# Kernel optimization log

Measured on AMD Instinct MI355X. Metric: run time of the kernel, lower is better.

## Reference

```python
import math
import jax, jax.numpy as jnp
import numpy as np

N_ORDERS = 2
CHUNK = 64  # tokens per chunk (before virtual-token expansion)


def _expand_derivative(x, n):
    """expand_virtual_tokens(mode='derivative'): [B,H,S,D] -> [B,H,S*n,D]."""
    B, H, S, D = x.shape
    pad = jnp.zeros((B, H, n - 1, D), x.dtype)
    xp = jnp.concatenate([pad, x], axis=2)  # [B,H,S+n-1,D]
    coeffs = np.array([(-1) ** kk * math.comb(n - 1, kk) for kk in range(n)], dtype=np.float32)
    coeffs = coeffs / np.abs(coeffs).sum()  # L1-normalized binomial coeffs
    # window j at token t is x_pad[t+j]*coeffs[j]; then flip window dim (as in torch .flip(-1))
    win = jnp.stack([xp[:, :, j:j + S, :] * coeffs[j] for j in range(n)], axis=3)  # [B,H,S,n,D]
    win = win[:, :, :, ::-1, :]
    return win.reshape(B, H, S * n, D)


def _unlinear(x, scale=2.0):
    """unlinear_activation: gated norm-scaled gelu applied to inter-chunk state."""
    xn = jnp.linalg.norm(x, axis=-1, keepdims=True) + 1e-6
    return x / scale * jax.nn.gelu(scale * x / xn, approximate=True)


def _stab(x):
    # ensure_stability: clamp to [-1e4, 1e4], nan -> center (0)
    return jnp.nan_to_num(jnp.clip(x, -1e4, 1e4), nan=0.0, posinf=1e4, neginf=-1e4)


def _forward(q, k, v, beta):
    n = N_ORDERS
    B, H, S, D = q.shape
    qe = _expand_derivative(q, n)
    ke = _expand_derivative(k, n)
    ve = _expand_derivative(v, n)
    be = jnp.repeat(beta, n, axis=-1)[..., None]  # [B,H,S*n,1]
    w = ke * be  # delta-rule write keys
    u = ve * be  # delta-rule write values

    Cn = CHUNK * n                     # virtual tokens per chunk
    NC = (S * n) // Cn                 # number of chunks
    ch = lambda x: x.reshape(B, H, NC, Cn, D)
    qc, kc, wc, uc = ch(qe), ch(ke), ch(w), ch(u)

    # triangular (forward-substitution) inversion per chunk:
    # T = (I + tril(W K^T, -1))^{-1}  == fast_invert_matrix of the strictly-lower system
    A = jnp.tril(jnp.einsum('bhnid,bhnjd->bhnij', wc, kc), -1)
    eye = jnp.eye(Cn, dtype=q.dtype)
    T = jax.scipy.linalg.solve_triangular(
        eye + A, jnp.broadcast_to(eye, A.shape), lower=True, unit_diagonal=True)
    wci = jnp.einsum('bhnij,bhnjd->bhnid', T, wc)
    uci = jnp.einsum('bhnij,bhnjd->bhnid', T, uc)

    def chunk_step(h, xs):
        # sequential_delta_product_scan body: per-token Householder updates, n_orders steps
        qx, wx, ux = xs  # each [B,H,Cn,D]
        C = CHUNK
        qr = qx.reshape(B, H, C, n, D)
        wr = wx.reshape(B, H, C, n, D)
        ur = ux.reshape(B, H, C, n, D)
        state = jnp.broadcast_to(h[:, :, None], (B, H, C, D, D))  # per-token state
        outs = []
        for s in range(n):
            qs, ws, us = qr[:, :, :, s], wr[:, :, :, s], ur[:, :, :, s]
            kho = jnp.einsum('bhcd,bhcde->bhce', ws, state)
            uval = us - kho
            o_inter = jnp.einsum('bhcd,bhcde->bhce', qs, state)
            o_intra = qs * uval
            state = _stab(state + jnp.einsum('bhcd,bhce->bhcde', ws, uval))
            outs.append(o_intra + o_inter)
        o = jnp.stack(outs, axis=3).reshape(B, H, C * n, D)  # interleave: pos t*n+s
        h_new = _unlinear(state[:, :, -1])  # linear_activation=False path
        return h_new, o

    xs = (jnp.moveaxis(qc, 2, 0), jnp.moveaxis(wci, 2, 0), jnp.moveaxis(uci, 2, 0))
    h0 = jnp.zeros((B, H, D, D), q.dtype)
    _, os = jax.lax.scan(chunk_step, h0, xs)  # os: [NC,B,H,Cn,D]
    out_v = jnp.moveaxis(os, 0, 2).reshape(B, H, S, n, D)
    return out_v[..., n - 1, :]  # collapse virtual tokens: keep last-order output per token


def setup_inputs() -> dict:
    key = jax.random.key(0)
    kq, kk, kv, kb = jax.random.split(key, 4)
    B, H, S, D = 2, 16, 2048, 64
    return {
        'q': jax.random.normal(kq, (B, H, S, D), jnp.float32),
        'k': jax.random.normal(kk, (B, H, S, D), jnp.float32),
        'v': jax.random.normal(kv, (B, H, S, D), jnp.float32),
        'beta': jax.random.uniform(kb, (B, H, S), jnp.float32),
    }


def reference(q, k, v, beta):
    return _forward(q, k, v, beta)
```

## Files before the change

kernel.cpp:

```cpp
#include <hip/hip_runtime.h>
#include <math.h>


namespace {
constexpr int PAIRS = 32;
constexpr int SLEN  = 2048;
constexpr int D     = 64;
constexpr int CK    = 64;
constexpr int CN    = 128;
constexpr int NCH   = 32;
constexpr int NB2   = 16;
constexpr int NP    = 5;
constexpr size_t YWORDS = (size_t)PAIRS * NCH * CN * CN;
constexpr int GP = 2145;
constexpr size_t GGW = (size_t)PAIRS * NCH * GP;
constexpr size_t HGW = (size_t)PAIRS * (NCH + 1) * D * D;
constexpr size_t FLW = PAIRS * NCH;

__device__ __forceinline__ float stab1(float x) {
    float y = __builtin_amdgcn_fmed3f(x, -10000.f, 10000.f);
    return (x != x) ? 0.f : y;
}
__device__ __forceinline__ int kidx(int a, int f4) {
    return a * 68 + 4 * (f4 ^ ((a >> 2) & 3));
}
__device__ __forceinline__ void bar_lds() {
    asm volatile("s_waitcnt lgkmcnt(0)\n\ts_barrier" ::: "memory");
}
}

__global__ __launch_bounds__(256, 2)
void la_gram(const float* __restrict__ kg, float* __restrict__ gG)
{
    __shared__ float kstf[65 * 68];
    const int blk = blockIdx.x;
    const int p = blk >> 5, nc = blk & 31;
    const int tid = threadIdx.x;
    const int baseT = nc * CK;
    const float* kp = kg + (size_t)p * SLEN * D;

    for (int u = tid; u < 65 * 16; u += 256) {
        int a = u >> 4, f4 = u & 15;
        int src = baseT - 1 + a;
        float4 val = float4{0.f, 0.f, 0.f, 0.f};
        if (src >= 0) val = ((const float4*)(kp + (size_t)src * D))[f4];
        *(float4*)&kstf[kidx(a, f4)] = val;
    }
    __syncthreads();

    float* gps = gG + (size_t)blk * GP;
    for (int tt = tid; tt < 17 * 17; tt += 256) {
        int ta = tt / 17, tb = tt % 17;
        if (tb > ta) continue;
        int a0 = ta * 4, b0 = tb * 4;
        float acc[4][4] = {};
        for (int d4 = 0; d4 < 16; ++d4) {
            float4 av[4], bv[4];
            #pragma unroll
            for (int r = 0; r < 4; ++r) {
                av[r] = *(const float4*)&kstf[kidx(min(a0 + r, 64), d4)];
                bv[r] = *(const float4*)&kstf[kidx(min(b0 + r, 64), d4)];
            }
            #pragma unroll
            for (int r = 0; r < 4; ++r)
                #pragma unroll
                for (int c = 0; c < 4; ++c)
                    acc[r][c] += av[r].x * bv[c].x + av[r].y * bv[c].y
                               + av[r].z * bv[c].z + av[r].w * bv[c].w;
        }
        #pragma unroll
        for (int r = 0; r < 4; ++r)
            #pragma unroll
            for (int c = 0; c < 4; ++c) {
                int a = a0 + r, b = b0 + c;
                if (a <= 64 && b <= a)
                    gps[a * (a + 1) / 2 + b] = acc[r][c];
            }
    }
}

__global__ __launch_bounds__(256, 3)
void la_p1scan(const float* __restrict__ kg, const float* __restrict__ vg,
               const float* __restrict__ bg, float* __restrict__ ws,
               const float* __restrict__ gG, float* __restrict__ hg,
               unsigned int* __restrict__ flags)
{
    __shared__ char shm[47808];
    const int blk = blockIdx.x;
    const int tid = threadIdx.x;

    if (blk < PAIRS) {
        float* w0s = (float*)shm;
        float* u0s = w0s + 64;
        float* w1s = u0s + 64;
        float* u1s = w1s + 64;
        float (*pA)[64] = (float(*)[64])(u1s + 64);
        float (*pB)[64] = pA + 4;
        float (*hsh2)[67] = (float(*)[67])(pB + 4);

        const int p = blk;
        const int w = tid >> 6, lane = tid & 63;
        const int hd = tid >> 2, he0 = (tid & 3) * 16;
        const float* Yp = ws + (size_t)p * NCH * (CN * CN);
        float* hp = hg + (size_t)p * (NCH + 1) * (D * D);
        const unsigned int* fl = (const unsigned int*)flags + (size_t)p * NCH;

        for (int idx = tid; idx < D * D; idx += 256) hp[idx] = 0.f;

        float hs[16];
        #pragma unroll
        for (int j = 0; j < 16; ++j) hs[j] = 0.f;

        for (int nc = 0; nc < NCH; ++nc) {
            if (tid == 0) {
                while (__hip_atomic_load(&fl[nc], __ATOMIC_ACQUIRE,
                                         __HIP_MEMORY_SCOPE_AGENT) < 2u)
                    __builtin_amdgcn_s_sleep(16);
            }
            __syncthreads();

            {
                float v = Yp[(size_t)nc * (CN * CN)
                             + (size_t)(126 + (tid >> 7)) * CN + (tid & 127)];
                if (tid < 64)       w0s[tid] = v;
                else if (tid < 128) u0s[tid - 64] = v;
                else if (tid < 192) w1s[tid - 128] = v;
                else                u1s[tid - 192] = v;
            }
            bar_lds();

            float s = 0.f;
            #pragma unroll
            for (int j = 0; j < 16; ++j) s += w0s[16 * w + j] * hs[j];
            pA[w][lane] = s;
            bar_lds();

            float sum = pA[0][lane] + pA[1][lane] + pA[2][lane] + pA[3][lane];
            const float uv0 = u0s[lane] - sum;

            float st1[16];
            float s2 = 0.f;
            #pragma unroll
            for (int j = 0; j < 16; ++j) {
                st1[j] = stab1(hs[j] + w0s[16 * w + j] * uv0);
                s2 += w1s[16 * w + j] * st1[j];
            }
            pB[w][lane] = s2;
            bar_lds();

            float sum2 = pB[0][lane] + pB[1][lane] + pB[2][lane] + pB[3][lane];
            const float uv1 = u1s[lane] - sum2;
            #pragma unroll
            for (int j = 0; j < 16; ++j)
                hsh2[16 * w + j][lane] = stab1(st1[j] + w1s[16 * w + j] * uv1);
            bar_lds();

            {
                float st2v[16];
                float ssum = 0.f;
                #pragma unroll
                for (int j = 0; j < 16; ++j) {
                    st2v[j] = hsh2[hd][he0 + j];
                    ssum += st2v[j] * st2v[j];
                }
                ssum += __shfl_xor(ssum, 1);
                ssum += __shfl_xor(ssum, 2);
                float xn = __builtin_amdgcn_sqrtf(ssum) + 1e-6f;
                float sc2 = 2.f * __builtin_amdgcn_rcpf(xn);
                float* ho = hp + (size_t)(nc + 1) * (D * D) + hd * 64 + he0;
                #pragma unroll
                for (int j4 = 0; j4 < 4; ++j4) {
                    float hn[4];
                    #pragma unroll
                    for (int q = 0; q < 4; ++q) {
                        float x  = st2v[4 * j4 + q];
                        float y  = x * sc2;
                        float y2 = y * y;
                        float e  = __builtin_amdgcn_exp2f(
                                       y * (2.3022078f + 0.1029432f * y2));
                        float th = (e - 1.f) * __builtin_amdgcn_rcpf(e + 1.f);
                        hn[q] = 0.25f * x * y * (1.f + th);
                        hsh2[hd][he0 + 4 * j4 + q] = hn[q];
                    }
                    *(float4*)&ho[4 * j4] = float4{hn[0], hn[1], hn[2], hn[3]};
                }
            }
            bar_lds();
            #pragma unroll
            for (int j = 0; j < 16; ++j) hs[j] = hsh2[16 * w + j][lane];
        }
        return;
    }

    float (*Ysh)[64]   = (float(*)[64])shm;
    float (*scm)[CN][8] = (float(*)[CN][8])(shm + 32768);
    float (*redsh)[66] = (float(*)[66])(shm + 40960);
    float* bq4 = (float*)(shm + 47296);
    float* bh  = bq4 + 64;

    const int idx  = blk - PAIRS;
    const int nc   = idx >> 6;
    const int p    = (idx & 63) >> 1;
    const int half = idx & 1;
    const int col  = tid & 63;
    const int m    = tid >> 6;
    const int baseT = nc * CK;
    const float* kp = kg + (size_t)p * SLEN * D;
    const float* vp = vg + (size_t)p * SLEN * D;
    const float* bp = bg + (size_t)p * SLEN;
    const float* gps = gG + (size_t)(p * NCH + nc) * GP;

    if (tid < CK) {
        float bv = bp[baseT + tid];
        bq4[tid] = 0.25f * bv;
        bh[tid]  = 0.5f  * bv;
    }
    __syncthreads();

    const float* srcBase = half ? vp : kp;
    for (int u = tid; u < CN * 16; u += 256) {
        int i = u >> 4, f4 = u & 15;
        int ci = i >> 1, si = i & 1;
        float sc = si ? bh[ci] : -bh[ci];
        int srcT = baseT + ci - si;
        float4 val = float4{0.f, 0.f, 0.f, 0.f};
        if (srcT >= 0) val = ((const float4*)(srcBase + (size_t)srcT * D))[f4];
        val.x *= sc; val.y *= sc; val.z *= sc; val.w *= sc;
        *(float4*)&Ysh[i][f4 * 4] = val;
    }
    for (int e = tid; e < 64; e += 256) {
        int j = e >> 3, r = e & 7;
        int ai = (r >> 1) - (r & 1) + 1;
        int aj = (j >> 1) - (j & 1) + 1;
        int amax = max(ai, aj), amin = min(ai, aj);
        float sgn = ((r ^ j) & 1) ? -1.f : 1.f;
        scm[0][j][r] = sgn * bq4[r >> 1] * gps[amax * (amax + 1) / 2 + amin];
    }
    __syncthreads();

    #pragma unroll
    for (int g = 0; g < 16; ++g) {
        const int buf = g & 1;
        float acc[8] = {};
        #pragma unroll
        for (int jj = 0; jj < 2 * g; ++jj) {
            const int j = m + 4 * jj;
            float yv = Ysh[j][col];
            const float4 a03 = *(const float4*)&scm[buf][j][0];
            const float4 a47 = *(const float4*)&scm[buf][j][4];
            acc[0] += a03.x * yv; acc[1] += a03.y * yv;
            acc[2] += a03.z * yv; acc[3] += a03.w * yv;
            acc[4] += a47.x * yv; acc[5] += a47.y * yv;
            acc[6] += a47.z * yv; acc[7] += a47.w * yv;
        }
        if (m > 0) {
            #pragma unroll
            for (int r = 0; r < 8; ++r) redsh[(m - 1) * 8 + r][col] = acc[r];
        }
        bar_lds();
        if (m == 0) {
            if (g > 0) {
                #pragma unroll
                for (int r = 0; r < 8; ++r)
                    acc[r] += redsh[r][col] + redsh[8 + r][col] + redsh[16 + r][col];
            }
            float yn[8];
            #pragma unroll
            for (int r = 0; r < 8; ++r) {
                float val = Ysh[8 * g + r][col] - acc[r];
                #pragma unroll
                for (int rp = 0; rp < 8; ++rp)
                    if (rp < r) val -= scm[buf][8 * g + rp][r] * yn[rp];
                yn[r] = val;
                Ysh[8 * g + r][col] = val;
            }
        } else if (g < 15) {
            const int T = g + 1, bufB = T & 1;
            const int nel = 8 * (8 * T + 8);
            constexpr int MAXIT = 6;
            const int nit = (nel + 191) / 192;
            #pragma unroll
            for (int it = 0; it < MAXIT; ++it) {
                if (it < nit) {
                    const int e = (tid - 64) + 192 * it;
                    if (e < nel) {
                        int j = e >> 3, r = e & 7;
                        int i = 8 * T + r;
                        int ai = (i >> 1) - (i & 1) + 1;
                        int aj = (j >> 1) - (j & 1) + 1;
                        int amax = max(ai, aj), amin = min(ai, aj);
                        float sgn = ((i ^ j) & 1) ? -1.f : 1.f;
                        scm[bufB][j][r] =
                            sgn * bq4[i >> 1] * gps[amax * (amax + 1) / 2 + amin];
                    }
                }
            }
        }
        bar_lds();
    }

    float* gY = ws + (size_t)(p * NCH + nc) * (CN * CN) + half * 64;
    for (int u = tid; u < CN * 16; u += 256) {
        int r = u >> 4, f4 = u & 15;
        *(float4*)&gY[r * CN + f4 * 4] = *(const float4*)&Ysh[r][f4 * 4];
    }
    __syncthreads();
    if (tid == 0)
        __hip_atomic_fetch_add(&flags[p * NCH + nc], 1u, __ATOMIC_RELEASE,
                               __HIP_MEMORY_SCOPE_AGENT);
}

__global__ __launch_bounds__(512)
void la_out(const float* __restrict__ qg, const float* __restrict__ ws,
            const float* __restrict__ hg, float* __restrict__ outg)
{
    __shared__ float hT[64 * 68];
    __shared__ float wbr[8][3][64];

    const int blk = blockIdx.x;
    const int p = blk >> 5, nc = blk & 31;
    const int tid = threadIdx.x;
    const int w = tid >> 6, lane = tid & 63;

    const float* Yc = ws + (size_t)(p * NCH + nc) * (CN * CN);
    const float* hp = hg + ((size_t)p * (NCH + 1) + nc) * (D * D);
    const float* qp = qg + (size_t)p * SLEN * D;
    float* op = outg + (size_t)p * SLEN * D;

    for (int idx = tid; idx < D * D; idx += 512) {
        int d = idx >> 6, e = idx & 63;
        hT[e * 68 + d] = hp[idx];
    }
    __syncthreads();

    float4 hr[16];
    #pragma unroll
    for (int k = 0; k < 16; ++k)
        hr[k] = *(const float4*)&hT[lane * 68 + 4 * k];

    float w0n, u0n, w1n, u1n, qn;
    {
        const int c = w, t = nc * CK + c;
        w0n = Yc[(size_t)(2 * c) * CN + lane];
        u0n = Yc[(size_t)(2 * c) * CN + 64 + lane];
        w1n = Yc[(size_t)(2 * c + 1) * CN + lane];
        u1n = Yc[(size_t)(2 * c + 1) * CN + 64 + lane];
        qn  = qp[(size_t)((t > 0) ? t - 1 : 0) * D + lane];
    }

    for (int it = 0; it < 8; ++it) {
        const int c = it * 8 + w;
        const int t = nc * CK + c;
        const float w0v = w0n, u0l = u0n, w1v = w1n, u1l = u1n, qv = qn;
        if (it < 7) {
            const int c2 = (it + 1) * 8 + w;
            w0n = Yc[(size_t)(2 * c2) * CN + lane];
            u0n = Yc[(size_t)(2 * c2) * CN + 64 + lane];
            w1n = Yc[(size_t)(2 * c2 + 1) * CN + lane];
            u1n = Yc[(size_t)(2 * c2 + 1) * CN + 64 + lane];
            qn  = qp[(size_t)(nc * CK + c2 - 1) * D + lane];
        }

        wbr[w][0][lane] = w0v;
        wbr[w][1][lane] = w1v;
        wbr[w][2][lane] = qv;

        float uv0 = u0l;
        #pragma unroll
        for (int k = 0; k < 16; ++k) {
            float4 wb = *(const float4*)&wbr[w][0][4 * k];
            uv0 -= (wb.x * hr[k].x + wb.y * hr[k].y)
                 + (wb.z * hr[k].z + wb.w * hr[k].w);
        }
        float kh = 0.f, oa = 0.f;
        #pragma unroll
        for (int k = 0; k < 16; ++k) {
            float4 wb0 = *(const float4*)&wbr[w][0][4 * k];
            float4 wb1 = *(const float4*)&wbr[w][1][4 * k];
            float4 qb  = *(const float4*)&wbr[w][2][4 * k];
            float st0 = stab1(hr[k].x + wb0.x * uv0);
            float st1 = stab1(hr[k].y + wb0.y * uv0);
            float st2 = stab1(hr[k].z + wb0.z * uv0);
            float st3 = stab1(hr[k].w + wb0.w * uv0);
            kh += (wb1.x * st0 + wb1.y * st1) + (wb1.z * st2 + wb1.w * st3);
            oa += (qb.x * st0 + qb.y * st1) + (qb.z * st2 + qb.w * st3);
        }
        float uv1 = u1l - kh;
        float outv = 0.5f * (qv * uv1 + oa);
        op[(size_t)t * D + lane] = (t > 0) ? outv : 0.f;
    }
}

__global__ __launch_bounds__(256, 3)
void la_phase1g(const float* __restrict__ kg, const float* __restrict__ vg,
                const float* __restrict__ bg, float* __restrict__ ws,
                const float* __restrict__ gG)
{
    __shared__ float Ysh[CN][64];
    __shared__ float scm[2][CN][8];
    __shared__ float redsh[24][66];
    __shared__ float bq4[CK], bh[CK];

    const int blk  = blockIdx.x;
    const int p    = blk >> 6;
    const int nc   = (blk >> 1) & 31;
    const int half = blk & 1;
    const int tid  = threadIdx.x;
    const int col  = tid & 63;
    const int m    = tid >> 6;
    const int baseT = nc * CK;
    const float* kp = kg + (size_t)p * SLEN * D;
    const float* vp = vg + (size_t)p * SLEN * D;
    const float* bp = bg + (size_t)p * SLEN;
    const float* gps = gG + (size_t)(p * NCH + nc) * GP;

    if (tid < CK) {
        float bv = bp[baseT + tid];
        bq4[tid] = 0.25f * bv;
        bh[tid]  = 0.5f  * bv;
    }
    __syncthreads();

    const float* srcBase = half ? vp : kp;
    for (int u = tid; u < CN * 16; u += 256) {
        int i = u >> 4, f4 = u & 15;
        int ci = i >> 1, si = i & 1;
        float sc = si ? bh[ci] : -bh[ci];
        int srcT = baseT + ci - si;
        float4 val = float4{0.f, 0.f, 0.f, 0.f};
        if (srcT >= 0) val = ((const float4*)(srcBase + (size_t)srcT * D))[f4];
        val.x *= sc; val.y *= sc; val.z *= sc; val.w *= sc;
        *(float4*)&Ysh[i][f4 * 4] = val;
    }
    for (int e = tid; e < 64; e += 256) {
        int j = e >> 3, r = e & 7;
        int ai = (r >> 1) - (r & 1) + 1;
        int aj = (j >> 1) - (j & 1) + 1;
        int amax = max(ai, aj), amin = min(ai, aj);
        float sgn = ((r ^ j) & 1) ? -1.f : 1.f;
        scm[0][j][r] = sgn * bq4[r >> 1] * gps[amax * (amax + 1) / 2 + amin];
    }
    __syncthreads();

    #pragma unroll
    for (int g = 0; g < 16; ++g) {
        const int buf = g & 1;
        float acc[8] = {};
        #pragma unroll
        for (int jj = 0; jj < 2 * g; ++jj) {
            const int j = m + 4 * jj;
            float yv = Ysh[j][col];
            const float4 a03 = *(const float4*)&scm[buf][j][0];
            const float4 a47 = *(const float4*)&scm[buf][j][4];
            acc[0] += a03.x * yv; acc[1] += a03.y * yv;
            acc[2] += a03.z * yv; acc[3] += a03.w * yv;
            acc[4] += a47.x * yv; acc[5] += a47.y * yv;
            acc[6] += a47.z * yv; acc[7] += a47.w * yv;
        }
        if (m > 0) {
            #pragma unroll
            for (int r = 0; r < 8; ++r) redsh[(m - 1) * 8 + r][col] = acc[r];
        }
        bar_lds();
        if (m == 0) {
            if (g > 0) {
                #pragma unroll
                for (int r = 0; r < 8; ++r)
                    acc[r] += redsh[r][col] + redsh[8 + r][col] + redsh[16 + r][col];
            }
            float yn[8];
            #pragma unroll
            for (int r = 0; r < 8; ++r) {
                float val = Ysh[8 * g + r][col] - acc[r];
                #pragma unroll
                for (int rp = 0; rp < 8; ++rp)
                    if (rp < r) val -= scm[buf][8 * g + rp][r] * yn[rp];
                yn[r] = val;
                Ysh[8 * g + r][col] = val;
            }
        } else if (g < 15) {
            const int T = g + 1, bufB = T & 1;
            const int nel = 8 * (8 * T + 8);
            constexpr int MAXIT = 6;
            const int nit = (nel + 191) / 192;
            #pragma unroll
            for (int it = 0; it < MAXIT; ++it) {
                if (it < nit) {
                    const int e = (tid - 64) + 192 * it;
                    if (e < nel) {
                        int j = e >> 3, r = e & 7;
                        int i = 8 * T + r;
                        int ai = (i >> 1) - (i & 1) + 1;
                        int aj = (j >> 1) - (j & 1) + 1;
                        int amax = max(ai, aj), amin = min(ai, aj);
                        float sgn = ((i ^ j) & 1) ? -1.f : 1.f;
                        scm[bufB][j][r] =
                            sgn * bq4[i >> 1] * gps[amax * (amax + 1) / 2 + amin];
                    }
                }
            }
        }
        bar_lds();
    }

    float* gY = ws + (size_t)(p * NCH + nc) * (CN * CN) + half * 64;
    for (int u = tid; u < CN * 16; u += 256) {
        int r = u >> 4, f4 = u & 15;
        *(float4*)&gY[r * CN + f4 * 4] = *(const float4*)&Ysh[r][f4 * 4];
    }
}

__global__ __launch_bounds__(512, 1)
void la_scan(const float* __restrict__ ws, float* __restrict__ hg)
{
    __shared__ float w0s[64], u0s[64], w1s[64], u1s[64];
    __shared__ float pA[8][64], pB[8][64];
    __shared__ float hsh2[64][67];

    const int p = blockIdx.x;
    const int tid = threadIdx.x;
    const int w = tid >> 6, lane = tid & 63;
    const int hd = tid >> 3, he0 = (tid & 7) * 8;
    const float* Yp = ws + (size_t)p * NCH * (CN * CN);
    float* hp = hg + (size_t)p * (NCH + 1) * (D * D);

    for (int idx = tid; idx < D * D; idx += 512) hp[idx] = 0.f;
    for (int idx = tid; idx < 64 * 67; idx += 512) (&hsh2[0][0])[idx] = 0.f;

    auto stagew = [&](float v) {
        if (tid < 64)       w0s[tid] = v;
        else if (tid < 128) u0s[tid - 64] = v;
        else if (tid < 192) w1s[tid - 128] = v;
        else if (tid < 256) u1s[tid - 192] = v;
    };
    {
        float v = 0.f;
        if (tid < 256) v = Yp[(size_t)(126 + (tid >> 7)) * CN + (tid & 127)];
        stagew(v);
    }
    float hs[8];
    #pragma unroll
    for (int j = 0; j < 8; ++j) hs[j] = 0.f;
    __syncthreads();

    for (int nc = 0; nc < NCH; ++nc) {
        float pf = 0.f;
        if (nc + 1 < NCH && tid < 256)
            pf = Yp[(size_t)(nc + 1) * (CN * CN)
                    + (size_t)(126 + (tid >> 7)) * CN + (tid & 127)];

        float s = 0.f;
        #pragma unroll
        for (int j = 0; j < 8; ++j) s += w0s[8 * w + j] * hs[j];
        pA[w][lane] = s;
        bar_lds();

        float sum = 0.f;
        #pragma unroll
        for (int wv = 0; wv < 8; ++wv) sum += pA[wv][lane];
        const float uv0 = u0s[lane] - sum;

        float st1[8];
        float s2 = 0.f;
        #pragma unroll
        for (int j = 0; j < 8; ++j) {
            st1[j] = stab1(hs[j] + w0s[8 * w + j] * uv0);
            s2 += w1s[8 * w + j] * st1[j];
        }
        pB[w][lane] = s2;
        bar_lds();

        float sum2 = 0.f;
        #pragma unroll
        for (int wv = 0; wv < 8; ++wv) sum2 += pB[wv][lane];
        const float uv1 = u1s[lane] - sum2;
        #pragma unroll
        for (int j = 0; j < 8; ++j)
            hsh2[8 * w + j][lane] = stab1(st1[j] + w1s[8 * w + j] * uv1);
        bar_lds();

        {
            float st2v[8];
            float ssum = 0.f;
            #pragma unroll
            for (int j = 0; j < 8; ++j) {
                st2v[j] = hsh2[hd][he0 + j];
                ssum += st2v[j] * st2v[j];
            }
            ssum += __shfl_xor(ssum, 1);
            ssum += __shfl_xor(ssum, 2);
            ssum += __shfl_xor(ssum, 4);
            float xn = __builtin_amdgcn_sqrtf(ssum) + 1e-6f;
            float sc2 = 2.f * __builtin_amdgcn_rcpf(xn);
            float hn[8];
            #pragma unroll
            for (int j = 0; j < 8; ++j) {
                float x  = st2v[j];
                float y  = x * sc2;
                float y2 = y * y;
                float e  = __builtin_amdgcn_exp2f(y * (2.3022078f + 0.1029432f * y2));
                float th = (e - 1.f) * __builtin_amdgcn_rcpf(e + 1.f);
                hn[j] = 0.25f * x * y * (1.f + th);
                hsh2[hd][he0 + j] = hn[j];
            }
            float* ho = hp + (size_t)(nc + 1) * (D * D) + hd * 64 + he0;
            *(float4*)&ho[0] = float4{hn[0], hn[1], hn[2], hn[3]};
            *(float4*)&ho[4] = float4{hn[4], hn[5], hn[6], hn[7]};
        }
        if (nc + 1 < NCH) stagew(pf);
        bar_lds();
        #pragma unroll
        for (int j = 0; j < 8; ++j) hs[j] = hsh2[8 * w + j][lane];
    }
}

__global__ __launch_bounds__(256, 2)
void la_phase1f(const float* __restrict__ kg, const float* __restrict__ vg,
                const float* __restrict__ bg, float* __restrict__ ws)
{
    __shared__ float Ysh[CN][64];
    __shared__ float Gm[65][66];
    __shared__ char  ureg[17680];
    __shared__ float bq4[CK], bh[CK];

    float* kstf = (float*)ureg;
    float* scm  = (float*)ureg;
    float (*redsh)[66] = (float(*)[66])(ureg + 8192);

    const int blk  = blockIdx.x;
    const int p    = blk >> 6;
    const int nc   = (blk >> 1) & 31;
    const int half = blk & 1;
    const int tid  = threadIdx.x;
    const int baseT = nc * CK;
    const float* kp = kg + (size_t)p * SLEN * D;
    const float* vp = vg + (size_t)p * SLEN * D;
    const float* bp = bg + (size_t)p * SLEN;

    for (int u = tid; u < 65 * 16; u += 256) {
        int a = u >> 4, f4 = u & 15;
        int src = baseT - 1 + a;
        float4 val = float4{0.f, 0.f, 0.f, 0.f};
        if (src >= 0) val = ((const float4*)(kp + (size_t)src * D))[f4];
        *(float4*)&kstf[kidx(a, f4)] = val;
    }
    if (tid < CK) {
        float bv = bp[baseT + tid];
        bq4[tid] = 0.25f * bv;
        bh[tid]  = 0.5f  * bv;
    }
    __syncthreads();

    for (int u = tid; u < CN * 16; u += 256) {
        int i = u >> 4, f4 = u & 15;
        int ci = i >> 1, si = i & 1;
        float sc = si ? bh[ci] : -bh[ci];
        float4 val = float4{0.f, 0.f, 0.f, 0.f};
        if (half == 0) {
            val = *(const float4*)&kstf[kidx(ci - si + 1, f4)];
        } else {
            int srcT = baseT + ci - si;
            if (srcT >= 0) val = ((const float4*)(vp + (size_t)srcT * D))[f4];
        }
        val.x *= sc; val.y *= sc; val.z *= sc; val.w *= sc;
        *(float4*)&Ysh[i][f4 * 4] = val;
    }

    for (int tt = tid; tt < 17 * 17; tt += 256) {
        int ta = tt / 17, tb = tt % 17;
        if (tb > ta) continue;
        int a0 = ta * 4, b0 = tb * 4;
        float acc[4][4] = {};
        for (int d4 = 0; d4 < 16; ++d4) {
            float4 av[4], bv[4];
            #pragma unroll
            for (int r = 0; r < 4; ++r) {
                av[r] = *(const float4*)&kstf[kidx(min(a0 + r, 64), d4)];
                bv[r] = *(const float4*)&kstf[kidx(min(b0 + r, 64), d4)];
            }
            #pragma unroll
            for (int r = 0; r < 4; ++r)
                #pragma unroll
                for (int c = 0; c < 4; ++c)
                    acc[r][c] += av[r].x * bv[c].x + av[r].y * bv[c].y
                               + av[r].z * bv[c].z + av[r].w * bv[c].w;
        }
        #pragma unroll
        for (int r = 0; r < 4; ++r)
            #pragma unroll
            for (int c = 0; c < 4; ++c)
                if (a0 + r <= 64 && b0 + c <= 64) {
                    Gm[a0 + r][b0 + c] = acc[r][c];
                    Gm[b0 + c][a0 + r] = acc[r][c];
                }
    }
    __syncthreads();

    auto stripf = [&](int g, int t0, int tstride) {
        int buf = g & 1;
        int jmax = 8 * g + 8;
        for (int e = t0; e < 8 * jmax; e += tstride) {
            int j = e >> 3, r = e & 7;
            int i = 8 * g + r;
            int ai = (i >> 1) - (i & 1) + 1;
            int aj = (j >> 1) - (j & 1) + 1;
            float sgn = ((i ^ j) & 1) ? -1.f : 1.f;
            scm[(buf * CN + j) * 8 + r] = sgn * bq4[i >> 1] * Gm[ai][aj];
        }
    };

    stripf(0, tid, 256);
    __syncthreads();

    const int col = tid & 63;
    const int m   = tid >> 6;
    for (int g = 0; g < 16; ++g) {
        const int buf = g & 1;
        float acc[8] = {};
        for (int j = m; j < 8 * g; j += 4) {
            float yv = Ysh[j][col];
            const float4 a03 = *(const float4*)&scm[(buf * CN + j) * 8];
            const float4 a47 = *(const float4*)&scm[(buf * CN + j) * 8 + 4];
            acc[0] += a03.x * yv; acc[1] += a03.y * yv;
            acc[2] += a03.z * yv; acc[3] += a03.w * yv;
            acc[4] += a47.x * yv; acc[5] += a47.y * yv;
            acc[6] += a47.z * yv; acc[7] += a47.w * yv;
        }
        if (m > 0) {
            #pragma unroll
            for (int r = 0; r < 8; ++r) redsh[(m - 1) * 8 + r][col] = acc[r];
        }
        __syncthreads();
        if (m == 0) {
            if (g > 0) {
                #pragma unroll
                for (int r = 0; r < 8; ++r)
                    acc[r] += redsh[r][col] + redsh[8 + r][col] + redsh[16 + r][col];
            }
            float yn[8];
            #pragma unroll
            for (int r = 0; r < 8; ++r) {
                float val = Ysh[8 * g + r][col] - acc[r];
                #pragma unroll
                for (int rp = 0; rp < 8; ++rp)
                    if (rp < r) val -= scm[(buf * CN + 8 * g + rp) * 8 + r] * yn[rp];
                yn[r] = val;
                Ysh[8 * g + r][col] = val;
            }
        } else if (g < 15) {
            stripf(g + 1, tid - 64, 192);
        }
        __syncthreads();
    }

    float* gY = ws + (size_t)(p * NCH + nc) * (CN * CN) + half * 64;
    for (int u = tid; u < CN * 16; u += 256) {
        int r = u >> 4, f4 = u & 15;
        *(float4*)&gY[r * CN + f4 * 4] = *(const float4*)&Ysh[r][f4 * 4];
    }
}

__global__ __launch_bounds__(512, 4)
void la_phase2(const float* __restrict__ qg, const float* __restrict__ ws,
               float* __restrict__ outg)
{
    __shared__ float WU[2][NP][256];
    __shared__ float Qs[2][NP][64];
    __shared__ float pR1[8][NP][64];
    __shared__ float pKH[8][NP][64];
    __shared__ float pOA[8][NP][64];
    __shared__ float UV0[NP][64];
    __shared__ float UV1r[64];
    __shared__ float hsh[64][67];

    const int blk  = blockIdx.x;
    const int p    = blk >> 4, nb = blk & 15;
    const int tid  = threadIdx.x;
    const int w    = tid >> 6, lane = tid & 63;
    const int hd   = tid >> 3;
    const int he0  = (tid & 7) * 8;

    const float* qp = qg + (size_t)p * SLEN * D;
    float* op = outg + (size_t)p * SLEN * D;
    const float* wsbase = ws + (size_t)p * NCH * (CN * CN);

    const int cMain = nb * 4 + w;

    float4 wuR = float4{0.f, 0.f, 0.f, 0.f};
    float  qR  = 0.f;

    auto stage_load = [&](int nc) {
        const float* gY = wsbase + (size_t)nc * (CN * CN);
        if (w < 4) {
            wuR = *(const float4*)(gY + (size_t)(2 * cMain) * CN + lane * 4);
            int t = nc * CK + cMain;
            qR = qp[(size_t)((t > 0) ? t - 1 : 0) * D + lane];
        } else if (w == 4) {
            wuR = *(const float4*)(gY + (size_t)126 * CN + lane * 4);
            qR = qp[(size_t)(nc * CK + 62) * D + lane];
        }
    };
    auto stage_write = [&](int buf) {
        if (w < NP) {
            *(float4*)&WU[buf][w][lane * 4] = wuR;
            Qs[buf][w][lane] = qR;
        }
    };

    for (int idx = tid; idx < 64 * 67; idx += 512) (&hsh[0][0])[idx] = 0.f;
    stage_load(0);
    stage_write(0);
    __syncthreads();

    for (int nc = 0; nc < NCH; ++nc) {
        const int buf = nc & 1;
        float hs[8];
        #pragma unroll
        for (int j = 0; j < 8; ++j) hs[j] = hsh[8 * w + j][lane];
        if (nc + 1 < NCH) stage_load(nc + 1);

        #pragma unroll
        for (int P = 0; P < NP; ++P) {
            float4 a = *(const float4*)&WU[buf][P][8 * w];
            float4 b = *(const float4*)&WU[buf][P][8 * w + 4];
            pR1[w][P][lane] =
                  ((a.x * hs[0] + a.y * hs[1]) + (a.z * hs[2] + a.w * hs[3]))
                + ((b.x * hs[4] + b.y * hs[5]) + (b.z * hs[6] + b.w * hs[7]));
        }
        __syncthreads();

        if (w < NP) {
            float s = 0.f;
            #pragma unroll
            for (int wv = 0; wv < 8; ++wv) s += pR1[wv][w][lane];
            UV0[w][lane] = WU[buf][w][64 + lane] - s;
        }
        __syncthreads();

        #pragma unroll
        for (int P = 0; P < NP; ++P) {
            float uv0 = UV0[P][lane];
            float4 w0a = *(const float4*)&WU[buf][P][8 * w];
            float4 w0b = *(const float4*)&WU[buf][P][8 * w + 4];
            float4 w1a = *(const float4*)&WU[buf][P][128 + 8 * w];
            float4 w1b = *(const float4*)&WU[buf][P][128 + 8 * w + 4];
            float4 qa  = *(const float4*)&Qs[buf][P][8 * w];
            float4 qb  = *(const float4*)&Qs[buf][P][8 * w + 4];
            float st0 = stab1(hs[0] + w0a.x * uv0);
            float st1 = stab1(hs[1] + w0a.y * uv0);
            float st2 = stab1(hs[2] + w0a.z * uv0);
            float st3 = stab1(hs[3] + w0a.w * uv0);
            float st4 = stab1(hs[4] + w0b.x * uv0);
            float st5 = stab1(hs[5] + w0b.y * uv0);
            float st6 = stab1(hs[6] + w0b.z * uv0);
            float st7 = stab1(hs[7] + w0b.w * uv0);
            pKH[w][P][lane] =
                  ((w1a.x * st0 + w1a.y * st1) + (w1a.z * st2 + w1a.w * st3))
                + ((w1b.x * st4 + w1b.y * st5) + (w1b.z * st6 + w1b.w * st7));
            pOA[w][P][lane] =
                  ((qa.x * st0 + qa.y * st1) + (qa.z * st2 + qa.w * st3))
                + ((qb.x * st4 + qb.y * st5) + (qb.z * st6 + qb.w * st7));
        }
        stage_write(buf ^ 1);
        __syncthreads();

        if (w < 4) {
            float skh = 0.f, soa = 0.f;
            #pragma unroll
            for (int wv = 0; wv < 8; ++wv) {
                skh += pKH[wv][w][lane];
                soa += pOA[wv][w][lane];
            }
            float uv1 = WU[buf][w][192 + lane] - skh;
            int t = nc * CK + cMain;
            float outv = 0.5f * (Qs[buf][w][lane] * uv1 + soa);
            op[(size_t)t * D + lane] = (t > 0) ? outv : 0.f;
        } else if (w == 4) {
            float skh = 0.f;
            #pragma unroll
            for (int wv = 0; wv < 8; ++wv) skh += pKH[wv][4][lane];
            UV1r[lane] = WU[buf][4][192 + lane] - skh;
        }
        __syncthreads();

        {
            float w0d = WU[buf][4][hd];
            float w1d = WU[buf][4][128 + hd];
            float st2v[8];
            float ssum = 0.f;
            #pragma unroll
            for (int j = 0; j < 8; ++j) {
                float st1 = stab1(hsh[hd][he0 + j] + w0d * UV0[4][he0 + j]);
                float st2 = stab1(st1 + w1d * UV1r[he0 + j]);
                st2v[j] = st2;
                ssum += st2 * st2;
            }
            ssum += __shfl_xor(ssum, 1);
            ssum += __shfl_xor(ssum, 2);
            ssum += __shfl_xor(ssum, 4);
            float xn = __builtin_amdgcn_sqrtf(ssum) + 1e-6f;
            float s2 = 2.f * __builtin_amdgcn_rcpf(xn);
            #pragma unroll
            for (int j = 0; j < 8; ++j) {
                float x  = st2v[j];
                float y  = x * s2;
                float y2 = y * y;
                float e  = __builtin_amdgcn_exp2f(y * (2.3022078f + 0.1029432f * y2));
                float th = (e - 1.f) * __builtin_amdgcn_rcpf(e + 1.f);
                hsh[hd][he0 + j] = 0.25f * x * y * (1.f + th);
            }
        }
        __syncthreads();
    }
}

extern "C" void kernel_launch(void* const* d_in, const int* in_sizes, int n_in,
                              void* d_out, int out_size, void* d_ws, size_t ws_size,
                              hipStream_t stream)
{
    (void)in_sizes; (void)n_in; (void)out_size;
    const float* q    = (const float*)d_in[0];
    const float* k    = (const float*)d_in[1];
    const float* v    = (const float*)d_in[2];
    const float* beta = (const float*)d_in[3];
    float* ws  = (float*)d_ws;
    float* out = (float*)d_out;

    const size_t maxW  = (HGW > GGW) ? HGW : GGW;
    const size_t needF = (YWORDS + GGW + HGW + FLW) * sizeof(float);
    const size_t needA = (YWORDS + maxW) * sizeof(float);
    const size_t needB = (YWORDS + GGW) * sizeof(float);

    if (ws_size >= needF) {
        float* gG = ws + YWORDS;
        float* hg = gG + GGW;
        unsigned int* flags = (unsigned int*)(hg + HGW);
        hipMemsetAsync(flags, 0, FLW * sizeof(unsigned int), stream);
        la_gram<<<PAIRS * NCH, 256, 0, stream>>>(k, gG);
        la_p1scan<<<PAIRS + PAIRS * NCH * 2, 256, 0, stream>>>(
            k, v, beta, ws, gG, hg, (unsigned int*)flags);
        la_out<<<PAIRS * NCH, 512, 0, stream>>>(q, ws, hg, out);
    } else if (ws_size >= needA) {
        float* gG = ws + YWORDS;
        float* hg = ws + YWORDS;
        la_gram<<<PAIRS * NCH, 256, 0, stream>>>(k, gG);
        la_phase1g<<<PAIRS * NCH * 2, 256, 0, stream>>>(k, v, beta, ws, gG);
        la_scan<<<PAIRS, 512, 0, stream>>>(ws, hg);
        la_out<<<PAIRS * NCH, 512, 0, stream>>>(q, ws, hg, out);
    } else if (ws_size >= needB) {
        float* gG = ws + YWORDS;
        la_gram<<<PAIRS * NCH, 256, 0, stream>>>(k, gG);
        la_phase1g<<<PAIRS * NCH * 2, 256, 0, stream>>>(k, v, beta, ws, gG);
        la_phase2<<<PAIRS * NB2, 512, 0, stream>>>(q, ws, out);
    } else {
        la_phase1f<<<PAIRS * NCH * 2, 256, 0, stream>>>(k, v, beta, ws);
        la_phase2<<<PAIRS * NB2, 512, 0, stream>>>(q, ws, out);
    }
}
```

Measured before the change: 292.7 us.

## Run inter-chunk scan in a single wavefront with readlane broadcasts

The sequential inter-chunk state scan in the fused kernel now runs on one 64-lane wavefront, with each lane holding a full 64-element column of the state in registers. The w/u vectors are broadcast with readlane instead of staged through LDS, and the four-wave partial sums and their block barriers are removed. The state is now stored transposed, so la_out's load and the fallback scan's store change to match. This shortens the serial critical path by dropping barriers, at the cost of fewer active lanes and heavy register pressure (64 floats of state per lane).

```diff
diff --git a/kernel.cpp b/kernel.cpp
--- a/kernel.cpp
+++ b/kernel.cpp
@@ -27,6 +27,9 @@
 __device__ __forceinline__ void bar_lds() {
     asm volatile("s_waitcnt lgkmcnt(0)\n\ts_barrier" ::: "memory");
 }
+__device__ __forceinline__ float rdlane(float v, int l) {
+    return __int_as_float(__builtin_amdgcn_readlane(__float_as_int(v), l));
+}
 }
 
 __global__ __launch_bounds__(256, 2)
@@ -90,104 +93,84 @@
     const int tid = threadIdx.x;
 
     if (blk < PAIRS) {
-        float* w0s = (float*)shm;
-        float* u0s = w0s + 64;
-        float* w1s = u0s + 64;
-        float* u1s = w1s + 64;
-        float (*pA)[64] = (float(*)[64])(u1s + 64);
-        float (*pB)[64] = pA + 4;
-        float (*hsh2)[67] = (float(*)[67])(pB + 4);
-
         const int p = blk;
-        const int w = tid >> 6, lane = tid & 63;
-        const int hd = tid >> 2, he0 = (tid & 3) * 16;
+        float* hp = hg + (size_t)p * (NCH + 1) * (D * D);
+        for (int idx = tid; idx < D * D; idx += 256) hp[idx] = 0.f;
+        if (tid >= 64) return;
+        const int lane = tid;
         const float* Yp = ws + (size_t)p * NCH * (CN * CN);
-        float* hp = hg + (size_t)p * (NCH + 1) * (D * D);
-        const unsigned int* fl = (const unsigned int*)flags + (size_t)p * NCH;
-
-        for (int idx = tid; idx < D * D; idx += 256) hp[idx] = 0.f;
-
-        float hs[16];
-        #pragma unroll
-        for (int j = 0; j < 16; ++j) hs[j] = 0.f;
+        const unsigned int* fl = flags + (size_t)p * NCH;
+        float* tr  = (float*)shm;
+        float* nsh = tr + 64 * 65;
+
+        float hs[64];
+        #pragma unroll
+        for (int d = 0; d < 64; ++d) hs[d] = 0.f;
 
         for (int nc = 0; nc < NCH; ++nc) {
-            if (tid == 0) {
-                while (__hip_atomic_load(&fl[nc], __ATOMIC_ACQUIRE,
-                                         __HIP_MEMORY_SCOPE_AGENT) < 2u)
-                    __builtin_amdgcn_s_sleep(16);
-            }
-            __syncthreads();
-
+            while (__hip_atomic_load(&fl[nc], __ATOMIC_ACQUIRE,
+                                     __HIP_MEMORY_SCOPE_AGENT) < 2u)
+                __builtin_amdgcn_s_sleep(8);
+            const float* Yc = Yp + (size_t)nc * (CN * CN);
+            const float w0v = Yc[126 * CN + lane];
+            const float u0v = Yc[126 * CN + 64 + lane];
+            const float w1v = Yc[127 * CN + lane];
+            const float u1v = Yc[127 * CN + 64 + lane];
+
+            float a0 = 0.f, a1 = 0.f, a2 = 0.f, a3 = 0.f;
+            #pragma unroll
+            for (int d = 0; d < 64; d += 4) {
+                a0 += rdlane(w0v, d)     * hs[d];
+                a1 += rdlane(w0v, d + 1) * hs[d + 1];
+                a2 += rdlane(w0v, d + 2) * hs[d + 2];
+                a3 += rdlane(w0v, d + 3) * hs[d + 3];
+            }
+            const float uv0 = u0v - ((a0 + a1) + (a2 + a3));
+
+            float b0 = 0.f, b1 = 0.f, b2 = 0.f, b3 = 0.f;
+            #pragma unroll
+            for (int d = 0; d < 64; d += 4) {
+                hs[d]     = stab1(hs[d]     + rdlane(w0v, d)     * uv0);
+                b0 += rdlane(w1v, d)     * hs[d];
+                hs[d + 1] = stab1(hs[d + 1] + rdlane(w0v, d + 1) * uv0);
+                b1 += rdlane(w1v, d + 1) * hs[d + 1];
+                hs[d + 2] = stab1(hs[d + 2] + rdlane(w0v, d + 2) * uv0);
+                b2 += rdlane(w1v, d + 2) * hs[d + 2];
+                hs[d + 3] = stab1(hs[d + 3] + rdlane(w0v, d + 3) * uv0);
+                b3 += rdlane(w1v, d + 3) * hs[d + 3];
+            }
+            const float uv1 = u1v - ((b0 + b1) + (b2 + b3));
+
+            #pragma unroll
+            for (int d = 0; d < 64; ++d)
+                hs[d] = stab1(hs[d] + rdlane(w1v, d) * uv1);
+
+            #pragma unroll
+            for (int d = 0; d < 64; ++d) tr[d * 65 + lane] = hs[d];
+            float ssum = 0.f;
+            #pragma unroll
+            for (int e = 0; e < 64; ++e) {
+                float v = tr[lane * 65 + e];
+                ssum += v * v;
+            }
             {
-                float v = Yp[(size_t)nc * (CN * CN)
-                             + (size_t)(126 + (tid >> 7)) * CN + (tid & 127)];
-                if (tid < 64)       w0s[tid] = v;
-                else if (tid < 128) u0s[tid - 64] = v;
-                else if (tid < 192) w1s[tid - 128] = v;
-                else                u1s[tid - 192] = v;
-            }
-            bar_lds();
-
-            float s = 0.f;
-            #pragma unroll
-            for (int j = 0; j < 16; ++j) s += w0s[16 * w + j] * hs[j];
-            pA[w][lane] = s;
-            bar_lds();
-
-            float sum = pA[0][lane] + pA[1][lane] + pA[2][lane] + pA[3][lane];
-            const float uv0 = u0s[lane] - sum;
-
-            float st1[16];
-            float s2 = 0.f;
-            #pragma unroll
-            for (int j = 0; j < 16; ++j) {
-                st1[j] = stab1(hs[j] + w0s[16 * w + j] * uv0);
-                s2 += w1s[16 * w + j] * st1[j];
-            }
-            pB[w][lane] = s2;
-            bar_lds();
-
-            float sum2 = pB[0][lane] + pB[1][lane] + pB[2][lane] + pB[3][lane];
-            const float uv1 = u1s[lane] - sum2;
-            #pragma unroll
-            for (int j = 0; j < 16; ++j)
-                hsh2[16 * w + j][lane] = stab1(st1[j] + w1s[16 * w + j] * uv1);
-            bar_lds();
-
-            {
-                float st2v[16];
-                float ssum = 0.f;
-                #pragma unroll
-                for (int j = 0; j < 16; ++j) {
-                    st2v[j] = hsh2[hd][he0 + j];
-                    ssum += st2v[j] * st2v[j];
-                }
-                ssum += __shfl_xor(ssum, 1);
-                ssum += __shfl_xor(ssum, 2);
                 float xn = __builtin_amdgcn_sqrtf(ssum) + 1e-6f;
-                float sc2 = 2.f * __builtin_amdgcn_rcpf(xn);
-                float* ho = hp + (size_t)(nc + 1) * (D * D) + hd * 64 + he0;
-                #pragma unroll
-                for (int j4 = 0; j4 < 4; ++j4) {
-                    float hn[4];
-                    #pragma unroll
-                    for (int q = 0; q < 4; ++q) {
-                        float x  = st2v[4 * j4 + q];
-                        float y  = x * sc2;
-                        float y2 = y * y;
-                        float e  = __builtin_amdgcn_exp2f(
-                                       y * (2.3022078f + 0.1029432f * y2));
-                        float th = (e - 1.f) * __builtin_amdgcn_rcpf(e + 1.f);
-                        hn[q] = 0.25f * x * y * (1.f + th);
-                        hsh2[hd][he0 + 4 * j4 + q] = hn[q];
-                    }
-                    *(float4*)&ho[4 * j4] = float4{hn[0], hn[1], hn[2], hn[3]};
-                }
-            }
-            bar_lds();
-            #pragma unroll
-            for (int j = 0; j < 16; ++j) hs[j] = hsh2[16 * w + j][lane];
+                nsh[lane] = 2.f * __builtin_amdgcn_rcpf(xn);
+            }
+            float* ho = hp + (size_t)(nc + 1) * (D * D) + (size_t)lane * 64;
+            #pragma unroll
+            for (int d = 0; d < 64; ++d) {
+                float x  = hs[d];
+                float y  = x * nsh[d];
+                float y2 = y * y;
+                float e  = __builtin_amdgcn_exp2f(y * (2.3022078f + 0.1029432f * y2));
+                float th = (e - 1.f) * __builtin_amdgcn_rcpf(e + 1.f);
+                hs[d] = 0.25f * x * y * (1.f + th);
+            }
+            #pragma unroll
+            for (int k = 0; k < 16; ++k)
+                *(float4*)&ho[4 * k] =
+                    float4{hs[4 * k], hs[4 * k + 1], hs[4 * k + 2], hs[4 * k + 3]};
         }
         return;
     }
@@ -327,10 +310,8 @@
     const float* qp = qg + (size_t)p * SLEN * D;
     float* op = outg + (size_t)p * SLEN * D;
 
-    for (int idx = tid; idx < D * D; idx += 512) {
-        int d = idx >> 6, e = idx & 63;
-        hT[e * 68 + d] = hp[idx];
-    }
+    for (int idx = tid; idx < D * D; idx += 512)
+        hT[(idx >> 6) * 68 + (idx & 63)] = hp[idx];
     __syncthreads();
 
     float4 hr[16];
@@ -592,7 +573,7 @@
             ssum += __shfl_xor(ssum, 4);
             float xn = __builtin_amdgcn_sqrtf(ssum) + 1e-6f;
             float sc2 = 2.f * __builtin_amdgcn_rcpf(xn);
-            float hn[8];
+            float* hob = hp + (size_t)(nc + 1) * (D * D);
             #pragma unroll
             for (int j = 0; j < 8; ++j) {
                 float x  = st2v[j];
@@ -600,12 +581,10 @@
                 float y2 = y * y;
                 float e  = __builtin_amdgcn_exp2f(y * (2.3022078f + 0.1029432f * y2));
                 float th = (e - 1.f) * __builtin_amdgcn_rcpf(e + 1.f);
-                hn[j] = 0.25f * x * y * (1.f + th);
-                hsh2[hd][he0 + j] = hn[j];
-            }
-            float* ho = hp + (size_t)(nc + 1) * (D * D) + hd * 64 + he0;
-            *(float4*)&ho[0] = float4{hn[0], hn[1], hn[2], hn[3]};
-            *(float4*)&ho[4] = float4{hn[4], hn[5], hn[6], hn[7]};
+                float hn = 0.25f * x * y * (1.f + th);
+                hsh2[hd][he0 + j] = hn;
+                hob[(size_t)(he0 + j) * 64 + hd] = hn;
+            }
         }
         if (nc + 1 < NCH) stagew(pf);
         bar_lds();
@@ -938,7 +917,7 @@
         hipMemsetAsync(flags, 0, FLW * sizeof(unsigned int), stream);
         la_gram<<<PAIRS * NCH, 256, 0, stream>>>(k, gG);
         la_p1scan<<<PAIRS + PAIRS * NCH * 2, 256, 0, stream>>>(
-            k, v, beta, ws, gG, hg, (unsigned int*)flags);
+            k, v, beta, ws, gG, hg, flags);
         la_out<<<PAIRS * NCH, 512, 0, stream>>>(q, ws, hg, out);
     } else if (ws_size >= needA) {
         float* gG = ws + YWORDS;
```

Measured after the change: 348.7 us. 1.19x slower.
